# Optimization experiments

Measured on AMD Instinct MI355X. Metric: run time of the kernel, lower is better.

The kernel has to match this reference:

```python
import jax, jax.numpy as jnp
import numpy as np

EPS = 1e-20
STRIDE, PADDING, DILATION = 1, 2, 1


def setup_inputs() -> dict:
    key = jax.random.key(0)
    ks = jax.random.split(key, 8)
    B, C, O, H, W, K = 8, 32, 32, 256, 256, 5
    return {
        "d": jax.random.uniform(ks[0], (B, C, H, W), jnp.float32) + 0.1,   # positive depth
        "cd": jax.random.uniform(ks[1], (B, C, H, W), jnp.float32),        # depth confidence in [0,1)
        "gx": jax.random.normal(ks[2], (B, C, H, W), jnp.float32),         # x-gradient
        "cgx": jax.random.uniform(ks[3], (B, C, H, W), jnp.float32),       # gradient confidence
        "w_prop": jax.random.normal(ks[4], (1, C, 1, 1), jnp.float32) * 0.1,
        "spatial_weight": jax.random.normal(ks[5], (C, 1, K, K), jnp.float32) * 0.1,
        "channel_weight": jax.random.normal(ks[6], (O, C, 1, 1), jnp.float32) * 0.1,
        "bias": jax.random.normal(ks[7], (1, O, 1, 1), jnp.float32) * 0.01,
    }


def _conv(x, w, groups, stride=1, padding=0, dilation=1):
    return jax.lax.conv_general_dilated(
        x, w, (stride, stride), ((padding, padding), (padding, padding)),
        rhs_dilation=(dilation, dilation),
        dimension_numbers=("NCHW", "OIHW", "NCHW"),
        feature_group_count=groups)


def reference(d, cd, gx, cgx, w_prop, spatial_weight, channel_weight, bias):
    in_channels = d.shape[1]
    # EnforcePos reparameterization: effective weights = softplus(raw)
    wp = jax.nn.softplus(w_prop)
    sw = jax.nn.softplus(spatial_weight)
    cw = jax.nn.softplus(channel_weight)

    pad_w = lambda x, lr: jnp.pad(x, ((0, 0), (0, 0), (0, 0), lr))
    d_left = pad_w(d[..., :-1], (0, 1))
    cd_left = pad_w(cd[..., :-1], (0, 1))
    d_right = pad_w(d[..., 1:], (1, 0))
    cd_right = pad_w(cd[..., 1:], (1, 0))

    cgx_from_ds = cd_left * cd_right
    height = (cd_left * d_left + cd_right * d_right) / (cd_left + cd_right + EPS)
    gx_from_ds = (d_right - d_left) / 2 / (height + EPS)

    gx_prop = (wp * cgx * gx + cgx_from_ds * gx_from_ds) / (wp * cgx + cgx_from_ds + EPS)
    cgx_prop = (wp * cgx + cgx_from_ds) / (wp + 1)

    # depthwise spatial conv (groups = in_channels), then 1x1 channel conv
    nom = _conv(cgx_prop * gx_prop, sw, in_channels, STRIDE, PADDING, DILATION)
    denom = _conv(cgx_prop, sw, in_channels, STRIDE, PADDING, DILATION)
    gx_s = nom / (denom + EPS)
    cgx_s = denom / jnp.sum(sw)

    nom = _conv(cgx_s * gx_s, cw, 1)
    denom = _conv(cgx_s, cw, 1)
    gx_out = nom / (denom + EPS) + bias
    cgx_out = denom / jnp.sum(cw)
    return (gx_out * STRIDE, cgx_out / (STRIDE * STRIDE))
```

## Files before the change

kernel.cpp:

```cpp
#include <hip/hip_runtime.h>
#include <math.h>

constexpr int IMG_H = 256;
constexpr int IMG_W = 256;
constexpr int NB = 8;
constexpr int NC = 32;
constexpr int NO = 32;
constexpr int PLANE = IMG_H * IMG_W;
constexpr int HALF = NB * NC * PLANE;

constexpr int TW = 16;
constexpr int TH = 32;
constexpr int NT = TW * TH;
constexpr int RR = TH + 4;
constexpr int RC = 24;
constexpr int RSB = RC * 8;
constexpr int BUFB = RR * RSB;
constexpr int NTASK = RR * 12;
constexpr int TILES = (IMG_W / TW) * (IMG_H / TH);

#define EPSV 1e-20f

typedef float f4 __attribute__((ext_vector_type(4)));
typedef float f2 __attribute__((ext_vector_type(2)));

__device__ __forceinline__ float rcpf_(float x) { return __builtin_amdgcn_rcpf(x); }
__device__ __forceinline__ float softplusf_(float x) {
  return fmaxf(x, 0.0f) + log1pf(expf(-fabsf(x)));
}

__global__ void weights_kernel(const float* __restrict__ wp_raw,
                               const float* __restrict__ sw_raw,
                               const float* __restrict__ cw_raw,
                               float* __restrict__ ws) {
  __shared__ float red[256];
  const int t = threadIdx.x;
  if (t < 32) ws[t] = softplusf_(wp_raw[t]);
  float ssum = 0.f;
  for (int i = t; i < NC * 25; i += 256) {
    float v = softplusf_(sw_raw[i]);
    ws[32 + i] = v;
    ssum += v;
  }
  float csum = 0.f;
  for (int i = t; i < NO * NC; i += 256) {
    float v = softplusf_(cw_raw[i]);
    int o = i >> 5, c = i & 31;
    ws[832 + c * NO + o] = v;
    csum += v;
  }
  red[t] = ssum; __syncthreads();
  for (int off = 128; off; off >>= 1) { if (t < off) red[t] += red[t + off]; __syncthreads(); }
  const float S_sw = red[0];
  __syncthreads();
  red[t] = csum; __syncthreads();
  for (int off = 128; off; off >>= 1) { if (t < off) red[t] += red[t + off]; __syncthreads(); }
  if (t == 0) { ws[1856] = S_sw; ws[1857] = red[0]; }
}

__device__ __forceinline__ void pointwise_pv(
    float dv, float cdv, float gxv, float cgv, int gw,
    float wpc, float inv_wp1, float& Pv, float& Vv) {
  float dl  = (gw == IMG_W - 1) ? 0.f : dv;
  float cdl = (gw == IMG_W - 1) ? 0.f : cdv;
  float dr  = (gw == 0) ? 0.f : dv;
  float cdr = (gw == 0) ? 0.f : cdv;
  float cfd = cdl * cdr;
  float height = (cdl * dl + cdr * dr) * rcpf_(cdl + cdr + EPSV);
  float gfd = (dr - dl) * 0.5f * rcpf_(height + EPSV);
  float den = fmaf(wpc, cgv, cfd);
  float num = fmaf(wpc * cgv, gxv, cfd * gfd);
  Pv = den * inv_wp1;
  Vv = num * inv_wp1;
}

__global__ __launch_bounds__(NT, 3) void fused_kernel(
    const float* __restrict__ dp, const float* __restrict__ cdp,
    const float* __restrict__ gxp, const float* __restrict__ cgxp,
    const float* __restrict__ ws, const float* __restrict__ bias,
    float* __restrict__ out) {
  __shared__ __align__(16) char shb[2 * BUFB];

  const int t = threadIdx.x;

  const int wg = blockIdx.x;
  const int virt = (wg & 7) * TILES + (wg >> 3);
  const int b = virt >> 7;
  const int tile = virt & (TILES - 1);
  const int tx = tile & 15, ty = tile >> 4;
  const int w0 = tx * TW, h0 = ty * TH;

  const float Ssw = ws[1856], Scw = ws[1857];
  const float epsS = EPSV * Ssw;
  const float oscale = rcpf_(Ssw) * rcpf_(Scw);

  const bool sact = t < NTASK;
  const int task = min(t, NTASK - 1);
  const int R = task / 12;
  const int hq = task - R * 12;
  const int gh = h0 + R - 2;
  const int ghc = min(max(gh, 0), IMG_H - 1);
  const int g0 = w0 - 4 + 2 * hq;
  const int g0c = min(max(g0, 0), IMG_W - 2);
  const int goff = ghc * IMG_W + g0c;
  const bool rowv = (unsigned)gh < (unsigned)IMG_H;
  const float m0 = (rowv & ((unsigned)g0 < (unsigned)IMG_W)) ? 1.f : 0.f;
  const float m1 = (rowv & ((unsigned)(g0 + 1) < (unsigned)IMG_W)) ? 1.f : 0.f;
  const int wb = R * RSB + hq * 16;

  const int x = t & (TW - 1);
  const int r = t >> 4;
  const int cvb = r * RSB + (x + 2) * 8;
  const int pixoff = (h0 + r) * IMG_W + (w0 + x);
  const int planebase = b * NC * PLANE;

  f2 accDN[32];
  #pragma unroll
  for (int o = 0; o < 32; ++o) accDN[o] = f2{0.f, 0.f};

  f2 vd, vc, vg, vx;
  if (sact) {
    vd = *(const f2*)(dp + planebase + goff);
    vc = *(const f2*)(cdp + planebase + goff);
    vg = *(const f2*)(gxp + planebase + goff);
    vx = *(const f2*)(cgxp + planebase + goff);
  }

  #pragma unroll 1
  for (int c = 0; c < NC; ++c) {
    char* buf = shb + (c & 1) * BUFB;
    const float wpc = ws[c];
    const float inv_wp1 = rcpf_(wpc + 1.0f);

    if (sact) {
      float P0, V0, P1, V1;
      pointwise_pv(vd[0], vc[0] * m0, vg[0], vx[0] * m0, g0,
                   wpc, inv_wp1, P0, V0);
      pointwise_pv(vd[1], vc[1] * m1, vg[1], vx[1] * m1, g0 + 1,
                   wpc, inv_wp1, P1, V1);
      f4 w; w[0] = P0; w[1] = V0; w[2] = P1; w[3] = V1;
      *(f4*)(buf + wb) = w;
    }

    __syncthreads();

    if ((c + 1 < NC) & sact) {
      const int pb = planebase + (c + 1) * PLANE + goff;
      vd = *(const f2*)(dp + pb);
      vc = *(const f2*)(cdp + pb);
      vg = *(const f2*)(gxp + pb);
      vx = *(const f2*)(cgxp + pb);
    }

    const char* bp = buf + cvb;
    const float* swc = ws + 32 + c * 25;
    f2 dn = f2{0.f, 0.f};
    #pragma unroll
    for (int kr = 0; kr < 5; ++kr) {
      #pragma unroll
      for (int kc = 0; kc < 5; ++kc) {
        const f2 pv = *(const f2*)(bp + kr * RSB + kc * 8);
        dn += pv * swc[kr * 5 + kc];
      }
    }

    const float* cwc = ws + 832 + c * NO;
    #pragma unroll
    for (int o = 0; o < 32; ++o)
      accDN[o] += dn * cwc[o];

  }

  const int ob = b * NO * PLANE + pixoff;
  #pragma unroll
  for (int o = 0; o < 32; ++o) {
    const float D = accDN[o][0], N = accDN[o][1];
    out[ob + o * PLANE] = fmaf(N, rcpf_(D + epsS), bias[o]);
    out[HALF + ob + o * PLANE] = D * oscale;
  }
}

extern "C" void kernel_launch(void* const* d_in, const int* in_sizes, int n_in,
                              void* d_out, int out_size, void* d_ws, size_t ws_size,
                              hipStream_t stream) {
  const float* dp   = (const float*)d_in[0];
  const float* cdp  = (const float*)d_in[1];
  const float* gxp  = (const float*)d_in[2];
  const float* cgxp = (const float*)d_in[3];
  const float* wp   = (const float*)d_in[4];
  const float* sw   = (const float*)d_in[5];
  const float* cw   = (const float*)d_in[6];
  const float* bias = (const float*)d_in[7];
  float* out = (float*)d_out;
  float* ws  = (float*)d_ws;

  weights_kernel<<<1, 256, 0, stream>>>(wp, sw, cw, ws);
  fused_kernel<<<TILES * NB, NT, 0, stream>>>(dp, cdp, gxp, cgxp, ws, bias,
                                              out);
}
```

Measured before the change: 396.7 us.

## Split output channels across thread pairs and stage four input channels per barrier

New measurement: 622.5 us. 1.57x slower.

```diff
diff --git a/kernel.cpp b/kernel.cpp
--- a/kernel.cpp
+++ b/kernel.cpp
@@ -10,14 +10,17 @@
 constexpr int HALF = NB * NC * PLANE;
 
 constexpr int TW = 16;
-constexpr int TH = 32;
-constexpr int NT = TW * TH;
-constexpr int RR = TH + 4;
+constexpr int TH = 16;
+constexpr int NT = 512;
+constexpr int RR = 20;
 constexpr int RC = 24;
 constexpr int RSB = RC * 8;
 constexpr int BUFB = RR * RSB;
 constexpr int NTASK = RR * 12;
+constexpr int CHPH = 4;
+constexpr int TPH = CHPH * NTASK;
 constexpr int TILES = (IMG_W / TW) * (IMG_H / TH);
+constexpr int NBLK = TILES * NB;
 
 #define EPSV 1e-20f
 
@@ -74,19 +77,43 @@
   Vv = num * inv_wp1;
 }
 
-__global__ __launch_bounds__(NT, 3) void fused_kernel(
+struct TaskGeo {
+  int goff;
+  int gc0;
+  float m0, m1;
+  int wb;
+};
+
+__device__ __forceinline__ TaskGeo make_geo(int inner, int h0, int w0) {
+  TaskGeo G;
+  const int R = inner / 12;
+  const int hq = inner - R * 12;
+  const int gh = h0 + R - 2;
+  const int ghc = min(max(gh, 0), IMG_H - 1);
+  const int g0 = w0 - 4 + 2 * hq;
+  const int g0c = min(max(g0, 0), IMG_W - 2);
+  G.goff = ghc * IMG_W + g0c;
+  G.gc0 = g0;
+  const bool rowv = (unsigned)gh < (unsigned)IMG_H;
+  G.m0 = (rowv & ((unsigned)g0 < (unsigned)IMG_W)) ? 1.f : 0.f;
+  G.m1 = (rowv & ((unsigned)(g0 + 1) < (unsigned)IMG_W)) ? 1.f : 0.f;
+  G.wb = R * RSB + hq * 16;
+  return G;
+}
+
+__global__ __launch_bounds__(NT, 5) void fused_kernel(
     const float* __restrict__ dp, const float* __restrict__ cdp,
     const float* __restrict__ gxp, const float* __restrict__ cgxp,
     const float* __restrict__ ws, const float* __restrict__ bias,
     float* __restrict__ out) {
-  __shared__ __align__(16) char shb[2 * BUFB];
+  __shared__ __align__(16) char shb[2 * CHPH * BUFB];
 
   const int t = threadIdx.x;
 
   const int wg = blockIdx.x;
-  const int virt = (wg & 7) * TILES + (wg >> 3);
-  const int b = virt >> 7;
-  const int tile = virt & (TILES - 1);
+  const int virt = (wg & 7) * (NBLK / 8) + (wg >> 3);
+  const int b = virt >> 8;
+  const int tile = virt & 255;
   const int tx = tile & 15, ty = tile >> 4;
   const int w0 = tx * TW, h0 = ty * TH;
 
@@ -94,89 +121,106 @@
   const float epsS = EPSV * Ssw;
   const float oscale = rcpf_(Ssw) * rcpf_(Scw);
 
-  const bool sact = t < NTASK;
-  const int task = min(t, NTASK - 1);
-  const int R = task / 12;
-  const int hq = task - R * 12;
-  const int gh = h0 + R - 2;
-  const int ghc = min(max(gh, 0), IMG_H - 1);
-  const int g0 = w0 - 4 + 2 * hq;
-  const int g0c = min(max(g0, 0), IMG_W - 2);
-  const int goff = ghc * IMG_W + g0c;
-  const bool rowv = (unsigned)gh < (unsigned)IMG_H;
-  const float m0 = (rowv & ((unsigned)g0 < (unsigned)IMG_W)) ? 1.f : 0.f;
-  const float m1 = (rowv & ((unsigned)(g0 + 1) < (unsigned)IMG_W)) ? 1.f : 0.f;
-  const int wb = R * RSB + hq * 16;
-
-  const int x = t & (TW - 1);
-  const int r = t >> 4;
-  const int cvb = r * RSB + (x + 2) * 8;
-  const int pixoff = (h0 + r) * IMG_W + (w0 + x);
+  const int c40 = t / NTASK;
+  const TaskGeo G0 = make_geo(t - c40 * NTASK, h0, w0);
+  const bool act1 = t < TPH - NT;
+  const int tk1 = min(t + NT, TPH - 1);
+  const int c41 = tk1 / NTASK;
+  const TaskGeo G1 = make_geo(tk1 - c41 * NTASK, h0, w0);
+
+  const int p = t >> 1;
+  const int og = t & 1;
+  const int x = p & 15, y = p >> 4;
+  const int cvb = y * RSB + (x + 2) * 8;
+  const int pixoff = (h0 + y) * IMG_W + (w0 + x);
   const int planebase = b * NC * PLANE;
 
-  f2 accDN[32];
+  f2 accDN[16];
   #pragma unroll
-  for (int o = 0; o < 32; ++o) accDN[o] = f2{0.f, 0.f};
-
-  f2 vd, vc, vg, vx;
-  if (sact) {
-    vd = *(const f2*)(dp + planebase + goff);
-    vc = *(const f2*)(cdp + planebase + goff);
-    vg = *(const f2*)(gxp + planebase + goff);
-    vx = *(const f2*)(cgxp + planebase + goff);
+  for (int o = 0; o < 16; ++o) accDN[o] = f2{0.f, 0.f};
+
+  f2 d0, c0, g0v, x0, d1, c1, g1v, x1;
+  {
+    const int p0 = planebase + c40 * PLANE + G0.goff;
+    d0 = *(const f2*)(dp + p0);  c0 = *(const f2*)(cdp + p0);
+    g0v = *(const f2*)(gxp + p0); x0 = *(const f2*)(cgxp + p0);
+    if (act1) {
+      const int p1 = planebase + c41 * PLANE + G1.goff;
+      d1 = *(const f2*)(dp + p1);  c1 = *(const f2*)(cdp + p1);
+      g1v = *(const f2*)(gxp + p1); x1 = *(const f2*)(cgxp + p1);
+    }
   }
 
   #pragma unroll 1
-  for (int c = 0; c < NC; ++c) {
-    char* buf = shb + (c & 1) * BUFB;
-    const float wpc = ws[c];
-    const float inv_wp1 = rcpf_(wpc + 1.0f);
-
-    if (sact) {
+  for (int ph = 0; ph < NC / CHPH; ++ph) {
+    const int cb = ph * CHPH;
+    char* bset = shb + (ph & 1) * CHPH * BUFB;
+
+    {
+      const float wpc = ws[cb + c40];
+      const float inv_wp1 = rcpf_(wpc + 1.0f);
       float P0, V0, P1, V1;
-      pointwise_pv(vd[0], vc[0] * m0, vg[0], vx[0] * m0, g0,
+      pointwise_pv(d0[0], c0[0] * G0.m0, g0v[0], x0[0] * G0.m0, G0.gc0,
                    wpc, inv_wp1, P0, V0);
-      pointwise_pv(vd[1], vc[1] * m1, vg[1], vx[1] * m1, g0 + 1,
+      pointwise_pv(d0[1], c0[1] * G0.m1, g0v[1], x0[1] * G0.m1, G0.gc0 + 1,
                    wpc, inv_wp1, P1, V1);
       f4 w; w[0] = P0; w[1] = V0; w[2] = P1; w[3] = V1;
-      *(f4*)(buf + wb) = w;
+      *(f4*)(bset + c40 * BUFB + G0.wb) = w;
+    }
+    if (act1) {
+      const float wpc = ws[cb + c41];
+      const float inv_wp1 = rcpf_(wpc + 1.0f);
+      float P0, V0, P1, V1;
+      pointwise_pv(d1[0], c1[0] * G1.m0, g1v[0], x1[0] * G1.m0, G1.gc0,
+                   wpc, inv_wp1, P0, V0);
+      pointwise_pv(d1[1], c1[1] * G1.m1, g1v[1], x1[1] * G1.m1, G1.gc0 + 1,
+                   wpc, inv_wp1, P1, V1);
+      f4 w; w[0] = P0; w[1] = V0; w[2] = P1; w[3] = V1;
+      *(f4*)(bset + c41 * BUFB + G1.wb) = w;
     }
 
     __syncthreads();
 
-    if ((c + 1 < NC) & sact) {
-      const int pb = planebase + (c + 1) * PLANE + goff;
-      vd = *(const f2*)(dp + pb);
-      vc = *(const f2*)(cdp + pb);
-      vg = *(const f2*)(gxp + pb);
-      vx = *(const f2*)(cgxp + pb);
-    }
-
-    const char* bp = buf + cvb;
-    const float* swc = ws + 32 + c * 25;
-    f2 dn = f2{0.f, 0.f};
+    if (ph + 1 < NC / CHPH) {
+      const int pb0 = planebase + (cb + CHPH + c40) * PLANE + G0.goff;
+      d0 = *(const f2*)(dp + pb0);  c0 = *(const f2*)(cdp + pb0);
+      g0v = *(const f2*)(gxp + pb0); x0 = *(const f2*)(cgxp + pb0);
+      if (act1) {
+        const int pb1 = planebase + (cb + CHPH + c41) * PLANE + G1.goff;
+        d1 = *(const f2*)(dp + pb1);  c1 = *(const f2*)(cdp + pb1);
+        g1v = *(const f2*)(gxp + pb1); x1 = *(const f2*)(cgxp + pb1);
+      }
+    }
+
+    __builtin_amdgcn_s_setprio(1);
     #pragma unroll
-    for (int kr = 0; kr < 5; ++kr) {
+    for (int cc = 0; cc < CHPH; ++cc) {
+      const char* bp = bset + cc * BUFB + cvb;
+      const float* swc = ws + 32 + (cb + cc) * 25;
+      f2 dn = f2{0.f, 0.f};
       #pragma unroll
-      for (int kc = 0; kc < 5; ++kc) {
-        const f2 pv = *(const f2*)(bp + kr * RSB + kc * 8);
-        dn += pv * swc[kr * 5 + kc];
+      for (int kr = 0; kr < 5; ++kr) {
+        #pragma unroll
+        for (int kc = 0; kc < 5; ++kc) {
+          const f2 pv = *(const f2*)(bp + kr * RSB + kc * 8);
+          dn += pv * swc[kr * 5 + kc];
+        }
       }
-    }
-
-    const float* cwc = ws + 832 + c * NO;
-    #pragma unroll
-    for (int o = 0; o < 32; ++o)
-      accDN[o] += dn * cwc[o];
-
+      const float* cwc = ws + 832 + (cb + cc) * NO + og * 16;
+      #pragma unroll
+      for (int o = 0; o < 16; ++o)
+        accDN[o] += dn * cwc[o];
+    }
+    __builtin_amdgcn_s_setprio(0);
   }
 
   const int ob = b * NO * PLANE + pixoff;
   #pragma unroll
-  for (int o = 0; o < 32; ++o) {
+  for (int o = 0; o < 16; ++o) {
+    const int oo = og * 16 + o;
     const float D = accDN[o][0], N = accDN[o][1];
-    out[ob + o * PLANE] = fmaf(N, rcpf_(D + epsS), bias[o]);
-    out[HALF + ob + o * PLANE] = D * oscale;
+    out[ob + oo * PLANE] = fmaf(N, rcpf_(D + epsS), bias[oo]);
+    out[HALF + ob + oo * PLANE] = D * oscale;
   }
 }
 
@@ -195,6 +239,5 @@
   float* ws  = (float*)d_ws;
 
   weights_kernel<<<1, 256, 0, stream>>>(wp, sw, cw, ws);
-  fused_kernel<<<TILES * NB, NT, 0, stream>>>(dp, cdp, gxp, cgxp, ws, bias,
-                                              out);
-}
+  fused_kernel<<<NBLK, NT, 0, stream>>>(dp, cdp, gxp, cgxp, ws, bias, out);
+}
```
